# Optimization experiments

Hardware: AMD Instinct MI355X
Metric: run time of the kernel (lower is better)

## Reference

```python
import jax, jax.numpy as jnp
import numpy as np

N_NODES = 100000


def gcn_conv(x, src, dst, ew, W, b, n_nodes):
    """PyG-style GCNConv: add self-loops, symmetric degree normalization,
    linear transform, scatter-add aggregation, bias."""
    loop = jnp.arange(n_nodes)
    src_f = jnp.concatenate([src, loop])          # [E+N]
    dst_f = jnp.concatenate([dst, loop])          # [E+N]
    ew_f = jnp.concatenate([ew, jnp.ones((n_nodes,), dtype=ew.dtype)])
    deg = jax.ops.segment_sum(ew_f, dst_f, num_segments=n_nodes)  # [N]
    dinv = jnp.where(deg > 0, jax.lax.rsqrt(deg), 0.0)
    norm = dinv[src_f] * ew_f * dinv[dst_f]       # [E+N]
    h = x @ W.T                                   # [N, out]
    msg = h[src_f] * norm[:, None]                # [E+N, out] gather + scale
    out = jax.ops.segment_sum(msg, dst_f, num_segments=n_nodes)
    return out + b


def prelu(x, a):
    return jnp.where(x >= 0, x, a * x)


def setup_inputs() -> dict:
    key = jax.random.key(0)
    k = jax.random.split(key, 8)
    in_c, out_c = 256, 128
    n_edges = 1600000
    x = jax.random.normal(k[0], (N_NODES, in_c), dtype=jnp.float32)
    edge_index = jax.random.randint(k[1], (2, n_edges), 0, N_NODES, dtype=jnp.int64)
    edge_weight = jax.random.uniform(k[2], (n_edges,), dtype=jnp.float32)
    W1 = jax.random.normal(k[3], (out_c, in_c), dtype=jnp.float32) / np.sqrt(in_c)
    b1 = jnp.zeros((out_c,), dtype=jnp.float32)
    W2 = jax.random.normal(k[4], (out_c, out_c), dtype=jnp.float32) / np.sqrt(out_c)
    b2 = jnp.zeros((out_c,), dtype=jnp.float32)
    a = jnp.asarray(0.25, dtype=jnp.float32)  # PReLU single shared parameter
    return {"x": x, "edge_index": edge_index, "edge_weight": edge_weight,
            "W1": W1, "b1": b1, "W2": W2, "b2": b2, "a": a}


def reference(x, edge_index, edge_weight, W1, b1, W2, b2, a):
    src, dst = edge_index[0], edge_index[1]
    h1 = prelu(gcn_conv(x, src, dst, edge_weight, W1, b1, N_NODES), a)
    h2 = prelu(gcn_conv(h1, src, dst, edge_weight, W2, b2, N_NODES), a)
    return (h1, h2)
```

## Files before the change

### kernel.cpp

```cpp
#include <hip/hip_runtime.h>


static __device__ __forceinline__ float4 ld4(const float* p) { return *(const float4*)p; }

static __device__ __forceinline__ unsigned short f2bf(float f) {
    unsigned u = __float_as_uint(f);
    u += 0x7fff + ((u >> 16) & 1);
    return (unsigned short)(u >> 16);
}
static __device__ __forceinline__ float bf2f(unsigned short h) {
    return __uint_as_float(((unsigned)h) << 16);
}

typedef __attribute__((ext_vector_type(8))) short short8v;
typedef __attribute__((ext_vector_type(4))) float f32x4;

static __device__ __forceinline__ int eidx(const void* ei, int flag, long long idx) {
    if (flag) return (int)((const long long*)ei)[idx];
    return ((const int*)ei)[idx];
}

__global__ void k_detect(const int* ei, int* flag) {
    __shared__ int anynz;
    if (threadIdx.x == 0) anynz = 0;
    __syncthreads();
    if (ei[2 * threadIdx.x + 1] != 0) anynz = 1;
    __syncthreads();
    if (threadIdx.x == 0) *flag = (anynz == 0) ? 1 : 0;
}

__global__ __launch_bounds__(256) void k_init(unsigned* packed, int N) {
    int i = blockIdx.x * 256 + threadIdx.x;
    if (i < N) packed[i] = 0u;
}

#define CNT_SH 24
#define DEG_SCALE 262144.0f
#define DEG_INV   3.814697265625e-06f

__global__ __launch_bounds__(256) void k_count(const void* __restrict__ ei,
                                               const float* __restrict__ ew,
                                               const int* __restrict__ flagp,
                                               unsigned* __restrict__ packed,
                                               int* __restrict__ rank, int E) {
    const int flag = *flagp;
    int base = blockIdx.x * 2048 + threadIdx.x;
    int d[8]; unsigned inc[8]; bool ok[8];
    #pragma unroll
    for (int u = 0; u < 8; ++u) {
        int e = base + u * 256;
        ok[u] = e < E;
        if (ok[u]) {
            d[u] = eidx(ei, flag, (long long)E + e);
            inc[u] = (1u << CNT_SH) | (unsigned)(ew[e] * DEG_SCALE);
        }
    }
    unsigned old[8];
    #pragma unroll
    for (int u = 0; u < 8; ++u)
        if (ok[u]) old[u] = atomicAdd(&packed[d[u]], inc[u]);
    #pragma unroll
    for (int u = 0; u < 8; ++u)
        if (ok[u]) rank[base + u * 256] = (int)(old[u] >> CNT_SH);
}

__global__ __launch_bounds__(256) void k_dinv(const unsigned* packed,
                                              float* dinv, int N) {
    int i = blockIdx.x * 256 + threadIdx.x;
    if (i < N) {
        float dg = 1.0f + (float)(packed[i] & 0xFFFFFFu) * DEG_INV;
        dinv[i] = rsqrtf(dg);
    }
}

__global__ __launch_bounds__(256) void k_blocksum(const unsigned* packed,
                                                  int* bsum, int N) {
    int i = blockIdx.x * 256 + threadIdx.x;
    int v = i < N ? (int)(packed[i] >> CNT_SH) : 0;
    for (int d = 32; d > 0; d >>= 1) v += __shfl_down(v, d, 64);
    __shared__ int wsum[4];
    int lane = threadIdx.x & 63, wid = threadIdx.x >> 6;
    if (lane == 0) wsum[wid] = v;
    __syncthreads();
    if (threadIdx.x == 0) bsum[blockIdx.x] = wsum[0] + wsum[1] + wsum[2] + wsum[3];
}

__global__ __launch_bounds__(512) void k_scan_bsum(int* bsum, int nb) {
    int t = threadIdx.x;
    int v = (t < nb) ? bsum[t] : 0;
    int orig = v;
    int lane = t & 63, wid = t >> 6;
    for (int d = 1; d < 64; d <<= 1) { int n = __shfl_up(v, d, 64); if (lane >= d) v += n; }
    __shared__ int wsum[8];
    if (lane == 63) wsum[wid] = v;
    __syncthreads();
    int woff = 0;
    for (int w = 0; w < 8; ++w) if (w < wid) woff += wsum[w];
    if (t < nb) bsum[t] = v - orig + woff;
}

__global__ __launch_bounds__(256) void k_scan_final(const unsigned* packed,
                                                    const int* bsum,
                                                    int* offs, int N, int E) {
    int b = blockIdx.x, t = threadIdx.x;
    int i = b * 256 + t;
    int v = (i < N) ? (int)(packed[i] >> CNT_SH) : 0;
    int orig = v;
    int lane = t & 63, wid = t >> 6;
    for (int d = 1; d < 64; d <<= 1) { int n = __shfl_up(v, d, 64); if (lane >= d) v += n; }
    __shared__ int wsum[4];
    if (lane == 63) wsum[wid] = v;
    __syncthreads();
    int woff = bsum[b];
    for (int w = 0; w < 4; ++w) if (w < wid) woff += wsum[w];
    if (i < N) offs[i] = v - orig + woff;
    if (i == 0) offs[N] = E;
}

__global__ __launch_bounds__(256) void k_scatter(const void* __restrict__ ei,
                                                 const float* __restrict__ ew,
                                                 const int* __restrict__ flagp,
                                                 const float* __restrict__ dinv,
                                                 const int* __restrict__ offs,
                                                 const int* __restrict__ rank,
                                                 int2* __restrict__ spair, int E) {
    const int flag = *flagp;
    int e = blockIdx.x * 256 + threadIdx.x;
    if (e < E) {
        int s = eidx(ei, flag, e);
        int d = eidx(ei, flag, (long long)E + e);
        int p = offs[d] + rank[e];
        float nrm = dinv[s] * ew[e] * dinv[d];
        int2 v; v.x = s; v.y = __float_as_int(nrm);
        spair[p] = v;
    }
}

template <int K>
__global__ __launch_bounds__(256) void k_packW(const float* __restrict__ W,
                                               unsigned short* __restrict__ Bp) {
    int t = blockIdx.x * 256 + threadIdx.x;
    if (t < 128 * K) {
        int col = t / K, k = t % K;
        int nt = col >> 4, ks = k >> 5;
        int lane = (col & 15) | (((k >> 3) & 3) << 4);
        int j = k & 7;
        Bp[(((size_t)nt * (K / 32) + ks) * 64 + lane) * 8 + j] = f2bf(W[t]);
    }
}

template <int K>
__global__ __launch_bounds__(128) void k_gemm(const float* __restrict__ X,
                                              const unsigned short* __restrict__ Bp,
                                              unsigned short* __restrict__ Hb,
                                              int M) {
    constexpr int KS = K / 32;
    int wave = threadIdx.x >> 6, lane = threadIdx.x & 63;
    int row0 = blockIdx.x * 64 + wave * 32;
    int r0 = row0 + (lane & 15);      if (r0 >= M) r0 = M - 1;
    int r1 = row0 + 16 + (lane & 15); if (r1 >= M) r1 = M - 1;
    int kc = (lane >> 4) * 8;
    const float* x0 = X + (size_t)r0 * K + kc;
    const float* x1 = X + (size_t)r1 * K + kc;

    f32x4 acc[2][8] = {};
    #pragma unroll 2
    for (int ks = 0; ks < KS; ++ks) {
        float4 a0 = ld4(x0 + ks * 32), a1 = ld4(x0 + ks * 32 + 4);
        float4 c0 = ld4(x1 + ks * 32), c1 = ld4(x1 + ks * 32 + 4);
        short8v af0, af1;
        af0[0] = (short)f2bf(a0.x); af0[1] = (short)f2bf(a0.y);
        af0[2] = (short)f2bf(a0.z); af0[3] = (short)f2bf(a0.w);
        af0[4] = (short)f2bf(a1.x); af0[5] = (short)f2bf(a1.y);
        af0[6] = (short)f2bf(a1.z); af0[7] = (short)f2bf(a1.w);
        af1[0] = (short)f2bf(c0.x); af1[1] = (short)f2bf(c0.y);
        af1[2] = (short)f2bf(c0.z); af1[3] = (short)f2bf(c0.w);
        af1[4] = (short)f2bf(c1.x); af1[5] = (short)f2bf(c1.y);
        af1[6] = (short)f2bf(c1.z); af1[7] = (short)f2bf(c1.w);
        #pragma unroll
        for (int nt = 0; nt < 8; ++nt) {
            short8v bf = *(const short8v*)&Bp[(((size_t)nt * KS + ks) * 64 + lane) * 8];
            acc[0][nt] = __builtin_amdgcn_mfma_f32_16x16x32_bf16(af0, bf, acc[0][nt], 0, 0, 0);
            acc[1][nt] = __builtin_amdgcn_mfma_f32_16x16x32_bf16(af1, bf, acc[1][nt], 0, 0, 0);
        }
    }
    #pragma unroll
    for (int rg = 0; rg < 2; ++rg) {
        int orow0 = row0 + rg * 16 + (lane >> 4) * 4;
        #pragma unroll
        for (int nt = 0; nt < 8; ++nt) {
            int col = nt * 16 + (lane & 15);
            #pragma unroll
            for (int j = 0; j < 4; ++j) {
                int r = orow0 + j;
                if (r < M) Hb[(size_t)r * 128 + col] = f2bf(acc[rg][nt][j]);
            }
        }
    }
}

__global__ __launch_bounds__(256) void k_agg(const unsigned short* __restrict__ Hb,
                                             const int* __restrict__ offs,
                                             const int2* __restrict__ spair,
                                             const float* __restrict__ dinv,
                                             const float* __restrict__ bias,
                                             const float* __restrict__ a_ptr,
                                             float* __restrict__ Out, int N) {
    int g = blockIdx.x * 8 + (threadIdx.x >> 5);
    int lane = threadIdx.x & 31;
    if (g >= N) return;
    float alpha = a_ptr[0];
    float di = dinv[g];
    float4 acc = ld4(bias + lane * 4);
    ushort4 hv = *(const ushort4*)(Hb + (size_t)g * 128 + lane * 4);
    float sw = di * di;
    acc.x += bf2f(hv.x) * sw; acc.y += bf2f(hv.y) * sw;
    acc.z += bf2f(hv.z) * sw; acc.w += bf2f(hv.w) * sw;
    int j0 = offs[g], j1 = offs[g + 1];
    for (int jb = j0; jb < j1; jb += 32) {
        int j = jb + lane;
        int s = 0; float w = 0.f;
        if (j < j1) { int2 sp = spair[j]; s = sp.x; w = __int_as_float(sp.y); }
        int cnt = j1 - jb; if (cnt > 32) cnt = 32;
        int full = cnt & ~3, i = 0;
        for (; i < full; i += 4) {
            int   s0 = __shfl(s, i,     32), s1 = __shfl(s, i + 1, 32);
            int   s2 = __shfl(s, i + 2, 32), s3 = __shfl(s, i + 3, 32);
            float w0 = __shfl(w, i,     32), w1 = __shfl(w, i + 1, 32);
            float w2 = __shfl(w, i + 2, 32), w3 = __shfl(w, i + 3, 32);
            ushort4 h0 = *(const ushort4*)(Hb + (size_t)s0 * 128 + lane * 4);
            ushort4 h1 = *(const ushort4*)(Hb + (size_t)s1 * 128 + lane * 4);
            ushort4 h2 = *(const ushort4*)(Hb + (size_t)s2 * 128 + lane * 4);
            ushort4 h3 = *(const ushort4*)(Hb + (size_t)s3 * 128 + lane * 4);
            acc.x += bf2f(h0.x) * w0; acc.y += bf2f(h0.y) * w0;
            acc.z += bf2f(h0.z) * w0; acc.w += bf2f(h0.w) * w0;
            acc.x += bf2f(h1.x) * w1; acc.y += bf2f(h1.y) * w1;
            acc.z += bf2f(h1.z) * w1; acc.w += bf2f(h1.w) * w1;
            acc.x += bf2f(h2.x) * w2; acc.y += bf2f(h2.y) * w2;
            acc.z += bf2f(h2.z) * w2; acc.w += bf2f(h2.w) * w2;
            acc.x += bf2f(h3.x) * w3; acc.y += bf2f(h3.y) * w3;
            acc.z += bf2f(h3.z) * w3; acc.w += bf2f(h3.w) * w3;
        }
        for (; i < cnt; ++i) {
            int   sv = __shfl(s, i, 32);
            float wv = __shfl(w, i, 32);
            ushort4 h4 = *(const ushort4*)(Hb + (size_t)sv * 128 + lane * 4);
            acc.x += bf2f(h4.x) * wv; acc.y += bf2f(h4.y) * wv;
            acc.z += bf2f(h4.z) * wv; acc.w += bf2f(h4.w) * wv;
        }
    }
    acc.x = acc.x >= 0.f ? acc.x : alpha * acc.x;
    acc.y = acc.y >= 0.f ? acc.y : alpha * acc.y;
    acc.z = acc.z >= 0.f ? acc.z : alpha * acc.z;
    acc.w = acc.w >= 0.f ? acc.w : alpha * acc.w;
    *(float4*)(Out + (size_t)g * 128 + lane * 4) = acc;
}

extern "C" void kernel_launch(void* const* d_in, const int* in_sizes, int n_in,
                              void* d_out, int out_size, void* d_ws, size_t ws_size,
                              hipStream_t stream) {
    const float* x  = (const float*)d_in[0];
    const void*  ei = d_in[1];
    const float* ew = (const float*)d_in[2];
    const float* W1 = (const float*)d_in[3];
    const float* b1 = (const float*)d_in[4];
    const float* W2 = (const float*)d_in[5];
    const float* b2 = (const float*)d_in[6];
    const float* ap = (const float*)d_in[7];
    const int N = in_sizes[0] / 256;
    const int E = in_sizes[2];

    float* out1 = (float*)d_out;
    float* out2 = out1 + (size_t)N * 128;

    char* p = (char*)d_ws;
    auto alloc = [&](size_t bytes) { void* r = (void*)p; p += (bytes + 255) & ~(size_t)255; return r; };
    unsigned* packed = (unsigned*)alloc((size_t)N * 4);
    float* dinv  = (float*)alloc((size_t)N * 4);
    int*   offs  = (int*)  alloc((size_t)(N + 1) * 4);
    int*   bsum  = (int*)  alloc((size_t)((N + 255) / 256) * 4);
    int*   flag  = (int*)  alloc(256);
    int*   rank  = (int*)  alloc((size_t)E * 4);
    int2*  spair = (int2*) alloc((size_t)E * 8);
    unsigned short* hb  = (unsigned short*)alloc((size_t)N * 128 * 2);
    unsigned short* bp1 = (unsigned short*)alloc((size_t)128 * 256 * 2);
    unsigned short* bp2 = (unsigned short*)alloc((size_t)128 * 128 * 2);

    const int nbN = (N + 255) / 256;
    const int nbE = (E + 255) / 256;
    const int nbE8 = (E + 2047) / 2048;

    k_detect<<<1, 256, 0, stream>>>((const int*)ei, flag);
    k_init<<<nbN, 256, 0, stream>>>(packed, N);
    k_packW<256><<<128, 256, 0, stream>>>(W1, bp1);
    k_packW<128><<<64, 256, 0, stream>>>(W2, bp2);
    k_count<<<nbE8, 256, 0, stream>>>(ei, ew, flag, packed, rank, E);
    k_blocksum<<<nbN, 256, 0, stream>>>(packed, bsum, N);
    k_scan_bsum<<<1, 512, 0, stream>>>(bsum, nbN);
    k_scan_final<<<nbN, 256, 0, stream>>>(packed, bsum, offs, N, E);
    k_dinv<<<nbN, 256, 0, stream>>>(packed, dinv, N);
    k_scatter<<<nbE, 256, 0, stream>>>(ei, ew, flag, dinv, offs, rank, spair, E);

    const int gb = (N + 63) / 64;
    k_gemm<256><<<gb, 128, 0, stream>>>(x, bp1, hb, N);
    k_agg<<<(N + 7) / 8, 256, 0, stream>>>(hb, offs, spair, dinv, b1, ap, out1, N);
    k_gemm<128><<<gb, 128, 0, stream>>>(out1, bp2, hb, N);
    k_agg<<<(N + 7) / 8, 256, 0, stream>>>(hb, offs, spair, dinv, b2, ap, out2, N);
}
```

Measured before the change: 315.4 us.

## Merge prep kernels and co-schedule edge counting with first GEMM

Combines init and both weight-packing kernels into one launch, runs the degree-count atomics and the first-layer GEMM as disjoint block ranges of a single kernel, and folds the dinv computation into the final scan. GEMM blocks now use 256 threads covering 128 rows. The aim is fewer kernel launches and overlap of the atomic-bound counting with the MFMA-bound GEMM. The cost is branch-divergent mixed kernels whose register and occupancy needs are set by the heavier GEMM path.

Result: faster. 306.9 us (-2.7%).

```diff
diff --git a/kernel.cpp b/kernel.cpp
--- a/kernel.cpp
+++ b/kernel.cpp
@@ -20,6 +20,10 @@
     return ((const int*)ei)[idx];
 }
 
+#define CNT_SH 24
+#define DEG_SCALE 262144.0f
+#define DEG_INV   3.814697265625e-06f
+
 __global__ void k_detect(const int* ei, int* flag) {
     __shared__ int anynz;
     if (threadIdx.x == 0) anynz = 0;
@@ -29,22 +33,43 @@
     if (threadIdx.x == 0) *flag = (anynz == 0) ? 1 : 0;
 }
 
-__global__ __launch_bounds__(256) void k_init(unsigned* packed, int N) {
-    int i = blockIdx.x * 256 + threadIdx.x;
-    if (i < N) packed[i] = 0u;
-}
-
-#define CNT_SH 24
-#define DEG_SCALE 262144.0f
-#define DEG_INV   3.814697265625e-06f
-
-__global__ __launch_bounds__(256) void k_count(const void* __restrict__ ei,
-                                               const float* __restrict__ ew,
-                                               const int* __restrict__ flagp,
-                                               unsigned* __restrict__ packed,
-                                               int* __restrict__ rank, int E) {
-    const int flag = *flagp;
-    int base = blockIdx.x * 2048 + threadIdx.x;
+static __device__ __forceinline__ void packW_body(const float* __restrict__ W,
+                                                  unsigned short* __restrict__ Bp,
+                                                  int t, int kbits) {
+    int K = 1 << kbits;
+    int col = t >> kbits, k = t & (K - 1);
+    int nt = col >> 4, ks = k >> 5;
+    int lane = (col & 15) | (((k >> 3) & 3) << 4);
+    int j = k & 7;
+    Bp[((((size_t)nt * (K >> 5) + ks) * 64 + lane) << 3) + j] = f2bf(W[t]);
+}
+
+__global__ __launch_bounds__(256) void k_prep(unsigned* __restrict__ packed, int N,
+                                              const float* __restrict__ W1,
+                                              unsigned short* __restrict__ bp1,
+                                              const float* __restrict__ W2,
+                                              unsigned short* __restrict__ bp2,
+                                              int nbInit) {
+    int b = blockIdx.x;
+    if (b < nbInit) {
+        int i = b * 256 + threadIdx.x;
+        if (i < N) packed[i] = 0u;
+    } else if (b < nbInit + 128) {
+        int t = (b - nbInit) * 256 + threadIdx.x;
+        packW_body(W1, bp1, t, 8);
+    } else {
+        int t = (b - nbInit - 128) * 256 + threadIdx.x;
+        packW_body(W2, bp2, t, 7);
+    }
+}
+
+static __device__ __forceinline__ void count_body(const void* __restrict__ ei,
+                                                  const float* __restrict__ ew,
+                                                  int flag,
+                                                  unsigned* __restrict__ packed,
+                                                  int* __restrict__ rank,
+                                                  int E, int cbid) {
+    int base = cbid * 2048 + threadIdx.x;
     int d[8]; unsigned inc[8]; bool ok[8];
     #pragma unroll
     for (int u = 0; u < 8; ++u) {
@@ -64,99 +89,14 @@
         if (ok[u]) rank[base + u * 256] = (int)(old[u] >> CNT_SH);
 }
 
-__global__ __launch_bounds__(256) void k_dinv(const unsigned* packed,
-                                              float* dinv, int N) {
-    int i = blockIdx.x * 256 + threadIdx.x;
-    if (i < N) {
-        float dg = 1.0f + (float)(packed[i] & 0xFFFFFFu) * DEG_INV;
-        dinv[i] = rsqrtf(dg);
-    }
-}
-
-__global__ __launch_bounds__(256) void k_blocksum(const unsigned* packed,
-                                                  int* bsum, int N) {
-    int i = blockIdx.x * 256 + threadIdx.x;
-    int v = i < N ? (int)(packed[i] >> CNT_SH) : 0;
-    for (int d = 32; d > 0; d >>= 1) v += __shfl_down(v, d, 64);
-    __shared__ int wsum[4];
-    int lane = threadIdx.x & 63, wid = threadIdx.x >> 6;
-    if (lane == 0) wsum[wid] = v;
-    __syncthreads();
-    if (threadIdx.x == 0) bsum[blockIdx.x] = wsum[0] + wsum[1] + wsum[2] + wsum[3];
-}
-
-__global__ __launch_bounds__(512) void k_scan_bsum(int* bsum, int nb) {
-    int t = threadIdx.x;
-    int v = (t < nb) ? bsum[t] : 0;
-    int orig = v;
-    int lane = t & 63, wid = t >> 6;
-    for (int d = 1; d < 64; d <<= 1) { int n = __shfl_up(v, d, 64); if (lane >= d) v += n; }
-    __shared__ int wsum[8];
-    if (lane == 63) wsum[wid] = v;
-    __syncthreads();
-    int woff = 0;
-    for (int w = 0; w < 8; ++w) if (w < wid) woff += wsum[w];
-    if (t < nb) bsum[t] = v - orig + woff;
-}
-
-__global__ __launch_bounds__(256) void k_scan_final(const unsigned* packed,
-                                                    const int* bsum,
-                                                    int* offs, int N, int E) {
-    int b = blockIdx.x, t = threadIdx.x;
-    int i = b * 256 + t;
-    int v = (i < N) ? (int)(packed[i] >> CNT_SH) : 0;
-    int orig = v;
-    int lane = t & 63, wid = t >> 6;
-    for (int d = 1; d < 64; d <<= 1) { int n = __shfl_up(v, d, 64); if (lane >= d) v += n; }
-    __shared__ int wsum[4];
-    if (lane == 63) wsum[wid] = v;
-    __syncthreads();
-    int woff = bsum[b];
-    for (int w = 0; w < 4; ++w) if (w < wid) woff += wsum[w];
-    if (i < N) offs[i] = v - orig + woff;
-    if (i == 0) offs[N] = E;
-}
-
-__global__ __launch_bounds__(256) void k_scatter(const void* __restrict__ ei,
-                                                 const float* __restrict__ ew,
-                                                 const int* __restrict__ flagp,
-                                                 const float* __restrict__ dinv,
-                                                 const int* __restrict__ offs,
-                                                 const int* __restrict__ rank,
-                                                 int2* __restrict__ spair, int E) {
-    const int flag = *flagp;
-    int e = blockIdx.x * 256 + threadIdx.x;
-    if (e < E) {
-        int s = eidx(ei, flag, e);
-        int d = eidx(ei, flag, (long long)E + e);
-        int p = offs[d] + rank[e];
-        float nrm = dinv[s] * ew[e] * dinv[d];
-        int2 v; v.x = s; v.y = __float_as_int(nrm);
-        spair[p] = v;
-    }
-}
-
 template <int K>
-__global__ __launch_bounds__(256) void k_packW(const float* __restrict__ W,
-                                               unsigned short* __restrict__ Bp) {
-    int t = blockIdx.x * 256 + threadIdx.x;
-    if (t < 128 * K) {
-        int col = t / K, k = t % K;
-        int nt = col >> 4, ks = k >> 5;
-        int lane = (col & 15) | (((k >> 3) & 3) << 4);
-        int j = k & 7;
-        Bp[(((size_t)nt * (K / 32) + ks) * 64 + lane) * 8 + j] = f2bf(W[t]);
-    }
-}
-
-template <int K>
-__global__ __launch_bounds__(128) void k_gemm(const float* __restrict__ X,
-                                              const unsigned short* __restrict__ Bp,
-                                              unsigned short* __restrict__ Hb,
-                                              int M) {
+static __device__ __forceinline__ void gemm_body(const float* __restrict__ X,
+                                                 const unsigned short* __restrict__ Bp,
+                                                 unsigned short* __restrict__ Hb,
+                                                 int M, int gbid) {
     constexpr int KS = K / 32;
     int wave = threadIdx.x >> 6, lane = threadIdx.x & 63;
-    int row0 = blockIdx.x * 64 + wave * 32;
+    int row0 = gbid * 128 + wave * 32;
     int r0 = row0 + (lane & 15);      if (r0 >= M) r0 = M - 1;
     int r1 = row0 + 16 + (lane & 15); if (r1 >= M) r1 = M - 1;
     int kc = (lane >> 4) * 8;
@@ -196,6 +136,95 @@
                 if (r < M) Hb[(size_t)r * 128 + col] = f2bf(acc[rg][nt][j]);
             }
         }
+    }
+}
+
+__global__ __launch_bounds__(256) void k_count_gemm1(
+        const void* __restrict__ ei, const float* __restrict__ ew,
+        const int* __restrict__ flagp, unsigned* __restrict__ packed,
+        int* __restrict__ rank, int E,
+        const float* __restrict__ X, const unsigned short* __restrict__ Bp,
+        unsigned short* __restrict__ Hb, int M, int nbCount) {
+    int b = blockIdx.x;
+    if (b < nbCount) {
+        count_body(ei, ew, *flagp, packed, rank, E, b);
+    } else {
+        gemm_body<256>(X, Bp, Hb, M, b - nbCount);
+    }
+}
+
+__global__ __launch_bounds__(256) void k_gemm2(const float* __restrict__ X,
+                                               const unsigned short* __restrict__ Bp,
+                                               unsigned short* __restrict__ Hb, int M) {
+    gemm_body<128>(X, Bp, Hb, M, blockIdx.x);
+}
+
+__global__ __launch_bounds__(256) void k_blocksum(const unsigned* packed,
+                                                  int* bsum, int N) {
+    int i = blockIdx.x * 256 + threadIdx.x;
+    int v = i < N ? (int)(packed[i] >> CNT_SH) : 0;
+    for (int d = 32; d > 0; d >>= 1) v += __shfl_down(v, d, 64);
+    __shared__ int wsum[4];
+    int lane = threadIdx.x & 63, wid = threadIdx.x >> 6;
+    if (lane == 0) wsum[wid] = v;
+    __syncthreads();
+    if (threadIdx.x == 0) bsum[blockIdx.x] = wsum[0] + wsum[1] + wsum[2] + wsum[3];
+}
+
+__global__ __launch_bounds__(512) void k_scan_bsum(int* bsum, int nb) {
+    int t = threadIdx.x;
+    int v = (t < nb) ? bsum[t] : 0;
+    int orig = v;
+    int lane = t & 63, wid = t >> 6;
+    for (int d = 1; d < 64; d <<= 1) { int n = __shfl_up(v, d, 64); if (lane >= d) v += n; }
+    __shared__ int wsum[8];
+    if (lane == 63) wsum[wid] = v;
+    __syncthreads();
+    int woff = 0;
+    for (int w = 0; w < 8; ++w) if (w < wid) woff += wsum[w];
+    if (t < nb) bsum[t] = v - orig + woff;
+}
+
+__global__ __launch_bounds__(256) void k_scan_final(const unsigned* packed,
+                                                    const int* bsum,
+                                                    int* offs, float* dinv,
+                                                    int N, int E) {
+    int b = blockIdx.x, t = threadIdx.x;
+    int i = b * 256 + t;
+    unsigned pk = (i < N) ? packed[i] : 0u;
+    int v = (int)(pk >> CNT_SH);
+    int orig = v;
+    int lane = t & 63, wid = t >> 6;
+    for (int d = 1; d < 64; d <<= 1) { int n = __shfl_up(v, d, 64); if (lane >= d) v += n; }
+    __shared__ int wsum[4];
+    if (lane == 63) wsum[wid] = v;
+    __syncthreads();
+    int woff = bsum[b];
+    for (int w = 0; w < 4; ++w) if (w < wid) woff += wsum[w];
+    if (i < N) {
+        offs[i] = v - orig + woff;
+        float dg = 1.0f + (float)(pk & 0xFFFFFFu) * DEG_INV;
+        dinv[i] = rsqrtf(dg);
+    }
+    if (i == 0) offs[N] = E;
+}
+
+__global__ __launch_bounds__(256) void k_scatter(const void* __restrict__ ei,
+                                                 const float* __restrict__ ew,
+                                                 const int* __restrict__ flagp,
+                                                 const float* __restrict__ dinv,
+                                                 const int* __restrict__ offs,
+                                                 const int* __restrict__ rank,
+                                                 int2* __restrict__ spair, int E) {
+    const int flag = *flagp;
+    int e = blockIdx.x * 256 + threadIdx.x;
+    if (e < E) {
+        int s = eidx(ei, flag, e);
+        int d = eidx(ei, flag, (long long)E + e);
+        int p = offs[d] + rank[e];
+        float nrm = dinv[s] * ew[e] * dinv[d];
+        int2 v; v.x = s; v.y = __float_as_int(nrm);
+        spair[p] = v;
     }
 }
 
@@ -286,24 +315,21 @@
     unsigned short* bp1 = (unsigned short*)alloc((size_t)128 * 256 * 2);
     unsigned short* bp2 = (unsigned short*)alloc((size_t)128 * 128 * 2);
 
-    const int nbN = (N + 255) / 256;
-    const int nbE = (E + 255) / 256;
-    const int nbE8 = (E + 2047) / 2048;
+    const int nbN    = (N + 255) / 256;
+    const int nbE    = (E + 255) / 256;
+    const int nbCnt  = (E + 2047) / 2048;
+    const int nbGemm = (N + 127) / 128;
 
     k_detect<<<1, 256, 0, stream>>>((const int*)ei, flag);
-    k_init<<<nbN, 256, 0, stream>>>(packed, N);
-    k_packW<256><<<128, 256, 0, stream>>>(W1, bp1);
-    k_packW<128><<<64, 256, 0, stream>>>(W2, bp2);
-    k_count<<<nbE8, 256, 0, stream>>>(ei, ew, flag, packed, rank, E);
+    k_prep<<<nbN + 128 + 64, 256, 0, stream>>>(packed, N, W1, bp1, W2, bp2, nbN);
+    k_count_gemm1<<<nbCnt + nbGemm, 256, 0, stream>>>(ei, ew, flag, packed, rank, E,
+                                                      x, bp1, hb, N, nbCnt);
     k_blocksum<<<nbN, 256, 0, stream>>>(packed, bsum, N);
     k_scan_bsum<<<1, 512, 0, stream>>>(bsum, nbN);
-    k_scan_final<<<nbN, 256, 0, stream>>>(packed, bsum, offs, N, E);
-    k_dinv<<<nbN, 256, 0, stream>>>(packed, dinv, N);
+    k_scan_final<<<nbN, 256, 0, stream>>>(packed, bsum, offs, dinv, N, E);
     k_scatter<<<nbE, 256, 0, stream>>>(ei, ew, flag, dinv, offs, rank, spair, E);
 
-    const int gb = (N + 63) / 64;
-    k_gemm<256><<<gb, 128, 0, stream>>>(x, bp1, hb, N);
     k_agg<<<(N + 7) / 8, 256, 0, stream>>>(hb, offs, spair, dinv, b1, ap, out1, N);
-    k_gemm<128><<<gb, 128, 0, stream>>>(out1, bp2, hb, N);
+    k_gemm2<<<nbGemm, 256, 0, stream>>>(out1, bp2, hb, N);
     k_agg<<<(N + 7) / 8, 256, 0, stream>>>(hb, offs, spair, dinv, b2, ap, out2, N);
 }
```
